# Kernel tuning notes

Measured on AMD Instinct MI355X. Metric: run time of the kernel, lower is better.

## Reference

```python
import jax, jax.numpy as jnp
from jax import lax
import numpy as np
import math

EPS = 1e-6

def _np(a, s=1.0):
    return np.asarray(a, dtype=np.float32) * np.float32(s)

def _gabor(theta, sigma=1.1, lambd=3.0, gamma=0.65):
    c = np.arange(-2, 3, dtype=np.float32)
    yy, xx = np.meshgrid(c, c, indexing='ij')
    xt = xx * math.cos(theta) + yy * math.sin(theta)
    yt = -xx * math.sin(theta) + yy * math.cos(theta)
    k = np.exp(-(xt**2 + gamma**2 * yt**2) / (2.0 * sigma**2)) * np.cos(2.0 * math.pi * xt / lambd)
    k = k - k.mean()
    return (k / max(np.abs(k).sum(), 1e-6)).astype(np.float32)

def _dct_like(u=2, v=2, size=5):
    c = np.arange(size, dtype=np.float32)
    yy, xx = np.meshgrid(c, c, indexing='ij')
    k = np.cos(math.pi*(2*xx+1)*u/(2*size)) * np.cos(math.pi*(2*yy+1)*v/(2*size))
    k = k - k.mean()
    return (k / max(np.abs(k).sum(), 1e-6)).astype(np.float32)

# stacked 3x3 stencils: laplacian, hess_xx, hess_yy, hess_xy, sobel_x, sobel_y, diag_main, diag_anti, checkerboard
_K3 = np.stack([
    _np([[0,1,0],[1,-4,1],[0,1,0]]),
    _np([[0,0,0],[1,-2,1],[0,0,0]]),
    _np([[0,1,0],[0,-2,0],[0,1,0]]),
    _np([[1,0,-1],[0,0,0],[-1,0,1]], 0.25),
    _np([[-1,0,1],[-2,0,2],[-1,0,1]], 0.125),
    _np([[-1,-2,-1],[0,0,0],[1,2,1]], 0.125),
    _np([[-2,-1,0],[-1,0,1],[0,1,2]], 0.125),
    _np([[0,1,2],[-1,0,1],[-2,-1,0]], 0.125),
    _np([[1,-1,1],[-1,1,-1],[1,-1,1]], 1.0/9.0),
])[:, None]

_Z5 = np.zeros((5,5), np.float32)

def _row5(vals):
    k = _Z5.copy(); k[2, :] = vals; return k

def _col5(vals):
    k = _Z5.copy(); k[:, 2] = vals; return k

# stacked 5x5 stencils: ha_second_h, ha_second_v, ha_green_h, ha_green_v, mhc_green, stripe_x, stripe_y, gabor45, gabor135, dct
_K5 = np.stack([
    _row5([-0.5, 0.0, 1.0, 0.0, -0.5]),
    _col5([-0.5, 0.0, 1.0, 0.0, -0.5]),
    _row5([-0.25, 0.5, 0.5, 0.5, -0.25]),
    _col5([-0.25, 0.5, 0.5, 0.5, -0.25]),
    _np([[0,0,-1,0,0],[0,0,2,0,0],[-1,2,4,2,-1],[0,0,2,0,0],[0,0,-1,0,0]], 0.125),
    _row5([0.25, -1.0, 1.5, -1.0, 0.25]),
    _col5([0.25, -1.0, 1.5, -1.0, 0.25]),
    _gabor(math.pi/4.0),
    _gabor(3.0*math.pi/4.0),
    _dct_like(),
])[:, None]

_SMOOTH5 = (_np([[1,2,3,2,1],[2,4,6,4,2],[3,6,9,6,3],[2,4,6,4,2],[1,2,3,2,1]]) / np.float32(81.0))[None, None]

K3 = jnp.asarray(_K3)
K5 = jnp.asarray(_K5)
SMOOTH5 = jnp.asarray(_SMOOTH5)

def _masks(H, W):
    # gbrg pattern
    z = lambda: np.zeros((1, 1, H, W), np.float32)
    r, b, gr, gb, row, col = z(), z(), z(), z(), z(), z()
    row[:, :, 1::2, :] = 1.0
    col[:, :, :, 1::2] = 1.0
    gb[:, :, 0::2, 0::2] = 1.0
    b[:, :, 0::2, 1::2] = 1.0
    r[:, :, 1::2, 0::2] = 1.0
    gr[:, :, 1::2, 1::2] = 1.0
    g = gr + gb
    return tuple(jnp.asarray(a) for a in (r, g, b, gr, gb, row, col))

def _pad(x, ph, pw):
    return jnp.pad(x, ((0, 0), (0, 0), (ph, ph), (pw, pw)), mode='reflect')

def _conv_same(x, k, groups=1):
    kh, kw = k.shape[-2:]
    return lax.conv_general_dilated(_pad(x, kh // 2, kw // 2), k.astype(x.dtype), (1, 1), 'VALID',
                                    dimension_numbers=('NCHW', 'OIHW', 'NCHW'),
                                    feature_group_count=groups)

def _avg_same(x, kh, kw):
    k = jnp.full((1, 1, kh, kw), 1.0 / (kh * kw), x.dtype)
    return _conv_same(x, k)

def _forward(bayer):
    B, _, H, W = bayer.shape
    r, g, b, gr, gb, row, col = _masks(H, W)
    c3 = _conv_same(bayer, K3)  # [B,9,H,W]
    lap, hxx, hyy, hxy, gx, gy, gdm, gda, chk = jnp.split(c3, 9, axis=1)
    c5 = _conv_same(bayer, K5)  # [B,10,H,W]
    hsh, hsv, hgh, hgv, mhcf, stx, sty, g45, g135, dctp = jnp.split(c5, 10, axis=1)
    # morphological gradient: 3x3 max - min (reflect-padded)
    xp = _pad(bayer, 1, 1)
    mgrad = (lax.reduce_window(xp, -jnp.inf, lax.max, (1, 1, 3, 3), (1, 1, 1, 1), 'VALID')
             - lax.reduce_window(xp, jnp.inf, lax.min, (1, 1, 3, 3), (1, 1, 1, 1), 'VALID'))
    gmag = jnp.sqrt(gx * gx + gy * gy + EPS)
    # structure tensor (3x3 box smoothing of gradient outer products)
    jxx = _avg_same(gx * gx, 3, 3)
    jyy = _avg_same(gy * gy, 3, 3)
    jxy = _avg_same(gx * gy, 3, 3)
    tr = jxx + jyy
    lam_gap = jnp.sqrt((jxx - jyy) ** 2 + 4.0 * jxy * jxy + EPS)
    coherence = lam_gap / (tr + EPS)
    anisotropy = (jxx - jyy) / (tr + EPS)
    ha_dis = jnp.abs(hgh - hgv)
    res_h = bayer - hgh
    res_v = bayer - hgv
    res_eh = _avg_same(res_h * res_h, 3, 3)
    res_ev = _avg_same(res_v * res_v, 3, 3)
    dgd = jnp.abs(gx) - jnp.abs(gy)
    dsd = jnp.abs(hxx) - jnp.abs(hyy)
    # 1x5 / 5x1 line variances
    mh = _avg_same(bayer, 1, 5)
    mv = _avg_same(bayer, 5, 1)
    lvh = jnp.maximum(_avg_same(bayer * bayer, 1, 5) - mh * mh, 0.0)
    lvv = jnp.maximum(_avg_same(bayer * bayer, 5, 1) - mv * mv, 0.0)
    lvd = lvh - lvv
    dconf = jnp.abs(lvd) / (lvh + lvv + EPS)
    # normalized sparse fills (smooth5 of masked signal / smooth5 of mask)
    mstack = jnp.concatenate([r, g, b, gr, gb], axis=1)  # [1,5,H,W]
    sig = bayer * mstack  # [B,5,H,W]
    ks = jnp.tile(SMOOTH5, (5, 1, 1, 1))
    num = _conv_same(sig, ks, groups=5)
    den = jnp.maximum(_conv_same(mstack, ks, groups=5), EPS)
    rf, gf, bf, grf, gbf = jnp.split(num / den, 5, axis=1)
    rg = rf - gf
    bg = bf - gf
    gpd = grf - gbf
    mhc = jnp.where(g > 0.5, bayer, mhcf)
    mhc_ha = mhc - 0.5 * (hgh + hgv)
    rres = (bayer - mhc) * r
    bres = (bayer - mhc) * b
    chk_e = _avg_same(chk * chk, 3, 3)
    str_e = _avg_same(stx * stx + sty * sty, 3, 3)
    lmean = _avg_same(bayer, 3, 3)
    lvar = jnp.maximum(_avg_same(bayer * bayer, 3, 3) - lmean * lmean, 0.0)
    gen = _avg_same(gx * gx + gy * gy, 3, 3)
    bm = lambda m: jnp.broadcast_to(m, bayer.shape)
    feats = [bm(r), bm(g), bm(b), bm(gr), bm(gb), bm(row), bm(col),
             lap, hxx, hyy, hxy, mgrad, gx, gy, gdm, gda, gmag,
             coherence, anisotropy, hsh, hsv, hgh, hgv, ha_dis,
             res_h, res_v, res_eh, res_ev, dgd, dsd, lvh, lvv, lvd, dconf,
             rg, bg, gpd, mhc, mhc_ha, rres, bres,
             stx, sty, chk, g45, g135, dctp, chk_e, str_e, lmean, lvar, gen]
    return jnp.concatenate(feats, axis=1)  # [B,52,H,W]

def setup_inputs() -> dict:
    key = jax.random.key(0)
    bayer = jax.random.uniform(key, (2, 1, 768, 768), dtype=jnp.float32)
    return {"bayer": bayer}

def reference(bayer):
    return _forward(bayer)
```

## Files before the change

### kernel.cpp

```cpp
#include <hip/hip_runtime.h>
#include <math.h>

#define H_ 768
#define W_ 768
#define TY 8
#define TX 64
#define NTHREADS 128
#define EPS_ 1e-6f

typedef float f4 __attribute__((ext_vector_type(4)));
typedef _Float16 h2 __attribute__((ext_vector_type(2)));

__device__ __forceinline__ f4 mk4(float x, float y, float z, float w){ f4 r; r.x=x; r.y=y; r.z=z; r.w=w; return r; }
__device__ __forceinline__ f4 sp(float s){ return mk4(s,s,s,s); }
__device__ __forceinline__ f4 max4(f4 a, f4 b){ return mk4(fmaxf(a.x,b.x),fmaxf(a.y,b.y),fmaxf(a.z,b.z),fmaxf(a.w,b.w)); }
__device__ __forceinline__ f4 sqrt4(f4 a){ return mk4(sqrtf(a.x),sqrtf(a.y),sqrtf(a.z),sqrtf(a.w)); }
__device__ __forceinline__ f4 abs4(f4 a){ return mk4(fabsf(a.x),fabsf(a.y),fabsf(a.z),fabsf(a.w)); }
__device__ __forceinline__ float rcp1(float x){
#if __has_builtin(__builtin_amdgcn_rcpf)
    return __builtin_amdgcn_rcpf(x);
#else
    return 1.0f / x;
#endif
}
__device__ __forceinline__ f4 rcp4(f4 a){ return mk4(rcp1(a.x),rcp1(a.y),rcp1(a.z),rcp1(a.w)); }
__device__ __forceinline__ h2 pk(float a, float b){ h2 r; r.x = (_Float16)a; r.y = (_Float16)b; return r; }

__device__ __forceinline__ int refl(int c, int n) {
    c = c < 0 ? -c : c;
    return c >= n ? 2 * n - 2 - c : c;
}

__global__ __launch_bounds__(NTHREADS, 4)
void bayer_feat(const float* __restrict__ in, float* __restrict__ out) {
    const int bz  = blockIdx.z;
    const int gy0 = blockIdx.y * TY;
    const int gx0 = blockIdx.x * TX;
    const int tid = threadIdx.x;
    const float* src = in + (size_t)bz * (H_ * W_);

    __shared__ float sB[TY + 6][TX + 7];
    __shared__ h2 sP[3][TY + 2][TX + 3];

    for (int i = tid; i < (TY + 6) * (TX + 6); i += NTHREADS) {
        int r = i / (TX + 6), c = i - r * (TX + 6);
        sB[r][c] = src[refl(gy0 - 3 + r, H_) * W_ + refl(gx0 - 3 + c, W_)];
    }
    __syncthreads();

    for (int i = tid; i < (TY + 2) * (TX + 2); i += NTHREADS) {
        int ey = i / (TX + 2), ex = i - ey * (TX + 2);
        int sy = refl(gy0 - 1 + ey, H_) - gy0 + 3;
        int sx = refl(gx0 - 1 + ex, W_) - gx0 + 3;
        float a00 = sB[sy-1][sx-1], a01 = sB[sy-1][sx], a02 = sB[sy-1][sx+1];
        float a10 = sB[sy  ][sx-1], a11 = sB[sy  ][sx], a12 = sB[sy  ][sx+1];
        float a20 = sB[sy+1][sx-1], a21 = sB[sy+1][sx], a22 = sB[sy+1][sx+1];
        float l2 = sB[sy][sx-2], r2 = sB[sy][sx+2];
        float u2 = sB[sy-2][sx], d2 = sB[sy+2][sx];
        float gx  = 0.125f * (-a00 + a02 - 2.f*a10 + 2.f*a12 - a20 + a22);
        float gy  = 0.125f * (-a00 - 2.f*a01 - a02 + a20 + 2.f*a21 + a22);
        float hgh = -0.25f*(l2 + r2) + 0.5f*(a10 + a11 + a12);
        float hgv = -0.25f*(u2 + d2) + 0.5f*(a01 + a11 + a21);
        float chk = (a00 - a01 + a02 - a10 + a11 - a12 + a20 - a21 + a22) * (1.f/9.f);
        float stx = 0.25f*(l2 + r2) - (a10 + a12) + 1.5f*a11;
        float sty = 0.25f*(u2 + d2) - (a01 + a21) + 1.5f*a11;
        float rh = a11 - hgh, rv = a11 - hgv;
        sP[0][ey][ex] = pk(gx, gy);
        sP[1][ey][ex] = pk(rh*rh, rv*rv);
        sP[2][ey][ex] = pk(chk*chk, stx*stx + sty*sty);
    }
    __syncthreads();

    const int lq  = tid & 15;
    const int ly  = tid >> 4;
    const int lx4 = lq * 4;
    const int gy  = gy0 + ly;
    const int py  = gy & 1;
    const int syc = ly + 3;
    const int ey  = ly + 1;
    const int exb = lx4 + 1;
    const size_t HW = (size_t)H_ * W_;
    float* po = out + (size_t)bz * 52 * HW + (size_t)gy * W_ + (gx0 + lx4);

#define ST(c, v) *(f4*)(po + (size_t)(c) * HW) = (v)
#define AV(r, i) mk4(a[r][i], a[r][(i)+1], a[r][(i)+2], a[r][(i)+3])

    const f4 zero4 = sp(0.f);
    const f4 ev01  = mk4(0,1,0,1);
    const f4 ev10  = mk4(1,0,1,0);
    const float inv9 = 1.f / 9.f;

    float a[5][8];
#pragma unroll
    for (int r = 0; r < 5; ++r)
#pragma unroll
        for (int i = 0; i < 8; ++i)
            a[r][i] = sB[syc - 2 + r][lx4 + 1 + i];


    {
        const float G45[5][5] = {
            {-0.002092f, -0.015195f, -0.063321f, -0.002285f,  0.036511f},
            {-0.015195f, -0.086304f,  0.003803f,  0.119456f, -0.002285f},
            {-0.063321f,  0.003803f,  0.172851f,  0.003803f, -0.063321f},
            {-0.002285f,  0.119456f,  0.003803f, -0.086304f, -0.015195f},
            { 0.036511f, -0.002285f, -0.063321f, -0.015195f, -0.002092f}
        };
        const float ADC[5] = {0.25f, -0.09549150f, -0.30901699f, -0.09549150f, 0.25f};
        f4 s45 = zero4, s135 = zero4, dct = zero4;
#pragma unroll
        for (int r = 0; r < 5; ++r) {
            f4 t = zero4;
#pragma unroll
            for (int i = 0; i < 5; ++i) {
                f4 v = AV(r, i);
                s45  += sp(G45[r][i])     * v;
                s135 += sp(G45[r][4 - i]) * v;
                t    += sp(ADC[i])        * v;
            }
            dct += sp(ADC[r]) * t;
        }
        ST(44, s45); ST(45, s135); ST(46, dct);
    }

    {
        f4 t0 = zero4, t1 = zero4, t2 = zero4, t3 = zero4;
#pragma unroll
        for (int r = 0; r < 5; ++r) {
            f4 E = AV(r,0) + sp(3.f)*AV(r,2) + AV(r,4);
            f4 O = sp(2.f)*(AV(r,1) + AV(r,3));
            f4 rE = mk4(E.x, O.y, E.z, O.w);
            f4 rO = mk4(O.x, E.y, O.z, E.w);
            if (r == 0 || r == 4)      { t0 += rE;          t2 += rO; }
            else if (r == 2)           { t0 += sp(3.f)*rE;  t2 += sp(3.f)*rO; }
            else                       { t1 += sp(2.f)*rE;  t3 += sp(2.f)*rO; }
        }
        f4 cEE = py ? t1 : t0, cOE = py ? t0 : t1, cEO = py ? t3 : t2, cOO = py ? t2 : t3;
        const f4 inv_r  = py ? mk4(0.04f,0.05f,0.04f,0.05f)     : mk4(0.05f,0.0625f,0.05f,0.0625f);
        const f4 inv_b  = py ? mk4(0.0625f,0.05f,0.0625f,0.05f) : mk4(0.05f,0.04f,0.05f,0.04f);
        const f4 inv_gr = py ? mk4(0.05f,0.04f,0.05f,0.04f)     : mk4(0.0625f,0.05f,0.0625f,0.05f);
        const f4 inv_gb = py ? mk4(0.05f,0.0625f,0.05f,0.0625f) : mk4(0.04f,0.05f,0.04f,0.05f);
        const f4 inv_g  = py ? mk4(1.f/40.f,1.f/41.f,1.f/40.f,1.f/41.f)
                             : mk4(1.f/41.f,1.f/40.f,1.f/41.f,1.f/40.f);
        f4 rfv = cOE*inv_r, bfv = cEO*inv_b, grfv = cOO*inv_gr, gbfv = cEE*inv_gb;
        f4 gfv = (cEE + cOO)*inv_g;
        ST(34, rfv - gfv); ST(35, bfv - gfv); ST(36, grfv - gbfv);
    }

    f4 ctr = AV(2,2);

    {
        f4 sh = AV(2,0)+AV(2,1)+ctr+AV(2,3)+AV(2,4);
        f4 qh = AV(2,0)*AV(2,0)+AV(2,1)*AV(2,1)+ctr*ctr+AV(2,3)*AV(2,3)+AV(2,4)*AV(2,4);
        f4 sv_ = AV(0,2)+AV(1,2)+ctr+AV(3,2)+AV(4,2);
        f4 qv_ = AV(0,2)*AV(0,2)+AV(1,2)*AV(1,2)+ctr*ctr+AV(3,2)*AV(3,2)+AV(4,2)*AV(4,2);
        f4 mh = sh * sp(0.2f), mv = sv_ * sp(0.2f);
        f4 lvh = max4(qh*sp(0.2f) - mh*mh, zero4);
        f4 lvv = max4(qv_*sp(0.2f) - mv*mv, zero4);
        ST(30, lvh); ST(31, lvv);
        f4 lvd = lvh - lvv;
        ST(32, lvd);
        ST(33, abs4(lvd) * rcp4(lvh + lvv + sp(EPS_)));
    }

    ST(19, sp(-0.5f)*(AV(2,0) + AV(2,4)) + ctr);
    ST(20, sp(-0.5f)*(AV(0,2) + AV(4,2)) + ctr);

    f4 hghc = sp(-0.25f)*(AV(2,0) + AV(2,4)) + sp(0.5f)*(AV(2,1) + ctr + AV(2,3));
    f4 hgvc = sp(-0.25f)*(AV(0,2) + AV(4,2)) + sp(0.5f)*(AV(1,2) + ctr + AV(3,2));
    {
        f4 mhcf = sp(0.125f)*( -AV(0,2) + sp(2.f)*AV(1,2) - AV(2,0) + sp(2.f)*AV(2,1) + sp(4.f)*ctr
                               + sp(2.f)*AV(2,3) - AV(2,4) + sp(2.f)*AV(3,2) - AV(4,2) );
        f4 mhc = py ? mk4(mhcf.x, ctr.y, mhcf.z, ctr.w) : mk4(ctr.x, mhcf.y, ctr.z, mhcf.w);
        ST(37, mhc);
        ST(38, mhc - sp(0.5f)*(hghc + hgvc));
        f4 dif = ctr - mhc;
        ST(39, dif * (py ? ev10 : zero4));
        ST(40, dif * (py ? zero4 : ev01));
    }
    ST(21, hghc); ST(22, hgvc);
    ST(23, abs4(hghc - hgvc));
    ST(24, ctr - hghc); ST(25, ctr - hgvc);

    {
        f4 gxc = sp(0.125f)*(-AV(1,1) + AV(1,3) - sp(2.f)*AV(2,1) + sp(2.f)*AV(2,3) - AV(3,1) + AV(3,3));
        f4 gyc = sp(0.125f)*(-AV(1,1) - sp(2.f)*AV(1,2) - AV(1,3) + AV(3,1) + sp(2.f)*AV(3,2) + AV(3,3));
        ST(12, gxc); ST(13, gyc);
        ST(16, sqrt4(gxc*gxc + gyc*gyc + sp(EPS_)));
        ST(28, abs4(gxc) - abs4(gyc));
    }
    {
        f4 stxc = sp(0.25f)*(AV(2,0) + AV(2,4)) - (AV(2,1) + AV(2,3)) + sp(1.5f)*ctr;
        f4 styc = sp(0.25f)*(AV(0,2) + AV(4,2)) - (AV(1,2) + AV(3,2)) + sp(1.5f)*ctr;
        f4 chkc = (AV(1,1) - AV(1,2) + AV(1,3) - AV(2,1) + ctr - AV(2,3) + AV(3,1) - AV(3,2) + AV(3,3)) * sp(inv9);
        ST(41, stxc); ST(42, styc); ST(43, chkc);
    }

    {
        f4 lap = AV(1,2) + AV(2,1) - sp(4.f)*ctr + AV(2,3) + AV(3,2);
        f4 hxx = AV(2,1) - sp(2.f)*ctr + AV(2,3);
        f4 hyy = AV(1,2) - sp(2.f)*ctr + AV(3,2);
        f4 hxy = sp(0.25f)*(AV(1,1) - AV(1,3) - AV(3,1) + AV(3,3));
        ST(7, lap); ST(8, hxx); ST(9, hyy); ST(10, hxy);
        ST(29, abs4(hxx) - abs4(hyy));
    }
    ST(14, sp(0.125f)*(sp(-2.f)*AV(1,1) - AV(1,2) - AV(2,1) + AV(2,3) + AV(3,2) + sp(2.f)*AV(3,3)));
    ST(15, sp(0.125f)*(AV(1,2) + sp(2.f)*AV(1,3) - AV(2,1) + AV(2,3) - sp(2.f)*AV(3,1) - AV(3,2)));

    {
        f4 mx = AV(1,1), mn = mx, s3 = zero4, q3 = zero4;
#pragma unroll
        for (int r = 1; r <= 3; ++r)
#pragma unroll
            for (int i = 1; i <= 3; ++i) {
                f4 v = AV(r,i);
                mx = max4(mx, v);
                mn = mk4(fminf(mn.x,v.x),fminf(mn.y,v.y),fminf(mn.z,v.z),fminf(mn.w,v.w));
                s3 += v; q3 += v*v;
            }
        ST(11, mx - mn);
        f4 lmean = s3 * sp(inv9);
        ST(49, lmean);
        ST(50, max4(q3*sp(inv9) - lmean*lmean, zero4));
    }

    {
        f4 jxx = zero4, jyy = zero4, jxy = zero4, reh = zero4, rev = zero4, cke = zero4, ste = zero4;
#pragma unroll
        for (int dy = -1; dy <= 1; ++dy) {
            float g_[6], h_[6];
#pragma unroll
            for (int j = 0; j < 6; ++j) {
                h2 v0 = sP[0][ey+dy][exb-1+j];
                g_[j] = (float)v0.x; h_[j] = (float)v0.y;
                h2 v1 = sP[1][ey+dy][exb-1+j];
                h2 v2 = sP[2][ey+dy][exb-1+j];
                (void)v1; (void)v2;
            }
#pragma unroll
            for (int o = 0; o < 3; ++o) {
                f4 q = mk4(g_[o], g_[o+1], g_[o+2], g_[o+3]);
                f4 w = mk4(h_[o], h_[o+1], h_[o+2], h_[o+3]);
                jxx += q*q; jyy += w*w; jxy += q*w;
            }
            float r2_[6], v2_[6], c2_[6], ss_[6];
#pragma unroll
            for (int j = 0; j < 6; ++j) {
                h2 v1 = sP[1][ey+dy][exb-1+j];
                r2_[j] = (float)v1.x; v2_[j] = (float)v1.y;
                h2 v2 = sP[2][ey+dy][exb-1+j];
                c2_[j] = (float)v2.x; ss_[j] = (float)v2.y;
            }
#pragma unroll
            for (int o = 0; o < 3; ++o) {
                reh += mk4(r2_[o], r2_[o+1], r2_[o+2], r2_[o+3]);
                rev += mk4(v2_[o], v2_[o+1], v2_[o+2], v2_[o+3]);
                cke += mk4(c2_[o], c2_[o+1], c2_[o+2], c2_[o+3]);
                ste += mk4(ss_[o], ss_[o+1], ss_[o+2], ss_[o+3]);
            }
        }
        jxx = jxx * sp(inv9); jyy = jyy * sp(inv9); jxy = jxy * sp(inv9);
        f4 trc = jxx + jyy;
        f4 dj  = jxx - jyy;
        f4 lam = sqrt4(dj*dj + sp(4.f)*jxy*jxy + sp(EPS_));
        f4 itr = rcp4(trc + sp(EPS_));
        ST(17, lam * itr);
        ST(18, dj * itr);
        ST(51, trc);
        ST(26, reh * sp(inv9)); ST(27, rev * sp(inv9));
        ST(47, cke * sp(inv9)); ST(48, ste * sp(inv9));
    }

    ST(0, py ? ev10 : zero4);
    ST(1, py ? ev01 : ev10);
    ST(2, py ? zero4 : ev01);
    ST(3, py ? ev01 : zero4);
    ST(4, py ? zero4 : ev10);
    ST(5, sp((float)py));
    ST(6, ev01);

#undef ST
#undef AV
}

extern "C" void kernel_launch(void* const* d_in, const int* in_sizes, int n_in,
                              void* d_out, int out_size, void* d_ws, size_t ws_size,
                              hipStream_t stream) {
    (void)n_in; (void)d_ws; (void)ws_size; (void)out_size;
    const float* bayer = (const float*)d_in[0];
    float* out = (float*)d_out;
    const int B = in_sizes[0] / (H_ * W_);
    dim3 grid(W_ / TX, H_ / TY, B);
    bayer_feat<<<grid, NTHREADS, 0, stream>>>(bayer, out);
}
```

Measured before the change: 47.53 us.

## Enlarge tile to 16x128 with 512 threads and vectorize shared-memory loads

Grows the block tile from 8x64 to 16x128 and the block from 128 to 512 threads, which cuts the fraction of halo pixels loaded and recomputed per output. Shared arrays are re-padded and offset so that 16-byte vector loads (f4 for the raw tile, h8 for the packed intermediates) are aligned, replacing scalar LDS reads. The larger block raises shared-memory use per block and may lower occupancy; launch_bounds still request 4 blocks per CU at 512 threads, which may constrain registers.

```diff
diff --git a/kernel.cpp b/kernel.cpp
--- a/kernel.cpp
+++ b/kernel.cpp
@@ -3,13 +3,17 @@
 
 #define H_ 768
 #define W_ 768
-#define TY 8
-#define TX 64
-#define NTHREADS 128
+#define TY 16
+#define TX 128
+#define NTHREADS 512
 #define EPS_ 1e-6f
+
+#define SBW 140
+#define SPW 132
 
 typedef float f4 __attribute__((ext_vector_type(4)));
 typedef _Float16 h2 __attribute__((ext_vector_type(2)));
+typedef _Float16 h8 __attribute__((ext_vector_type(8)));
 
 __device__ __forceinline__ f4 mk4(float x, float y, float z, float w){ f4 r; r.x=x; r.y=y; r.z=z; r.w=w; return r; }
 __device__ __forceinline__ f4 sp(float s){ return mk4(s,s,s,s); }
@@ -39,19 +43,19 @@
     const int tid = threadIdx.x;
     const float* src = in + (size_t)bz * (H_ * W_);
 
-    __shared__ float sB[TY + 6][TX + 7];
-    __shared__ h2 sP[3][TY + 2][TX + 3];
+    __shared__ __align__(16) float sB[TY + 6][SBW];
+    __shared__ __align__(16) h2 sP[3][TY + 2][SPW];
 
     for (int i = tid; i < (TY + 6) * (TX + 6); i += NTHREADS) {
         int r = i / (TX + 6), c = i - r * (TX + 6);
-        sB[r][c] = src[refl(gy0 - 3 + r, H_) * W_ + refl(gx0 - 3 + c, W_)];
+        sB[r][c + 3] = src[refl(gy0 - 3 + r, H_) * W_ + refl(gx0 - 3 + c, W_)];
     }
     __syncthreads();
 
     for (int i = tid; i < (TY + 2) * (TX + 2); i += NTHREADS) {
         int ey = i / (TX + 2), ex = i - ey * (TX + 2);
         int sy = refl(gy0 - 1 + ey, H_) - gy0 + 3;
-        int sx = refl(gx0 - 1 + ex, W_) - gx0 + 3;
+        int sx = refl(gx0 - 1 + ex, W_) - gx0 + 6;
         float a00 = sB[sy-1][sx-1], a01 = sB[sy-1][sx], a02 = sB[sy-1][sx+1];
         float a10 = sB[sy  ][sx-1], a11 = sB[sy  ][sx], a12 = sB[sy  ][sx+1];
         float a20 = sB[sy+1][sx-1], a21 = sB[sy+1][sx], a22 = sB[sy+1][sx+1];
@@ -71,14 +75,13 @@
     }
     __syncthreads();
 
-    const int lq  = tid & 15;
-    const int ly  = tid >> 4;
+    const int lq  = tid & 31;
+    const int ly  = tid >> 5;
     const int lx4 = lq * 4;
     const int gy  = gy0 + ly;
     const int py  = gy & 1;
     const int syc = ly + 3;
     const int ey  = ly + 1;
-    const int exb = lx4 + 1;
     const size_t HW = (size_t)H_ * W_;
     float* po = out + (size_t)bz * 52 * HW + (size_t)gy * W_ + (gx0 + lx4);
 
@@ -92,10 +95,12 @@
 
     float a[5][8];
 #pragma unroll
-    for (int r = 0; r < 5; ++r)
-#pragma unroll
-        for (int i = 0; i < 8; ++i)
-            a[r][i] = sB[syc - 2 + r][lx4 + 1 + i];
+    for (int r = 0; r < 5; ++r) {
+        f4 lo = *(const f4*)&sB[syc - 2 + r][lx4 + 4];
+        f4 hi = *(const f4*)&sB[syc - 2 + r][lx4 + 8];
+        a[r][0]=lo.x; a[r][1]=lo.y; a[r][2]=lo.z; a[r][3]=lo.w;
+        a[r][4]=hi.x; a[r][5]=hi.y; a[r][6]=hi.z; a[r][7]=hi.w;
+    }
 
 
     {
@@ -228,31 +233,34 @@
         f4 jxx = zero4, jyy = zero4, jxy = zero4, reh = zero4, rev = zero4, cke = zero4, ste = zero4;
 #pragma unroll
         for (int dy = -1; dy <= 1; ++dy) {
-            float g_[6], h_[6];
-#pragma unroll
-            for (int j = 0; j < 6; ++j) {
-                h2 v0 = sP[0][ey+dy][exb-1+j];
-                g_[j] = (float)v0.x; h_[j] = (float)v0.y;
-                h2 v1 = sP[1][ey+dy][exb-1+j];
-                h2 v2 = sP[2][ey+dy][exb-1+j];
-                (void)v1; (void)v2;
+            const int ry = ey + dy;
+            float g_[6], h_[6], r2_[6], v2_[6], c2_[6], ss_[6];
+            {
+                const h8 e = *(const h8*)&sP[0][ry][lx4];
+                g_[0]=e[0]; h_[0]=e[1]; g_[1]=e[2]; h_[1]=e[3];
+                g_[2]=e[4]; h_[2]=e[5]; g_[3]=e[6]; h_[3]=e[7];
+                h2 a4 = sP[0][ry][lx4+4], a5 = sP[0][ry][lx4+5];
+                g_[4]=a4.x; h_[4]=a4.y; g_[5]=a5.x; h_[5]=a5.y;
+            }
+            {
+                const h8 e = *(const h8*)&sP[1][ry][lx4];
+                r2_[0]=e[0]; v2_[0]=e[1]; r2_[1]=e[2]; v2_[1]=e[3];
+                r2_[2]=e[4]; v2_[2]=e[5]; r2_[3]=e[6]; v2_[3]=e[7];
+                h2 a4 = sP[1][ry][lx4+4], a5 = sP[1][ry][lx4+5];
+                r2_[4]=a4.x; v2_[4]=a4.y; r2_[5]=a5.x; v2_[5]=a5.y;
+            }
+            {
+                const h8 e = *(const h8*)&sP[2][ry][lx4];
+                c2_[0]=e[0]; ss_[0]=e[1]; c2_[1]=e[2]; ss_[1]=e[3];
+                c2_[2]=e[4]; ss_[2]=e[5]; c2_[3]=e[6]; ss_[3]=e[7];
+                h2 a4 = sP[2][ry][lx4+4], a5 = sP[2][ry][lx4+5];
+                c2_[4]=a4.x; ss_[4]=a4.y; c2_[5]=a5.x; ss_[5]=a5.y;
             }
 #pragma unroll
             for (int o = 0; o < 3; ++o) {
                 f4 q = mk4(g_[o], g_[o+1], g_[o+2], g_[o+3]);
                 f4 w = mk4(h_[o], h_[o+1], h_[o+2], h_[o+3]);
                 jxx += q*q; jyy += w*w; jxy += q*w;
-            }
-            float r2_[6], v2_[6], c2_[6], ss_[6];
-#pragma unroll
-            for (int j = 0; j < 6; ++j) {
-                h2 v1 = sP[1][ey+dy][exb-1+j];
-                r2_[j] = (float)v1.x; v2_[j] = (float)v1.y;
-                h2 v2 = sP[2][ey+dy][exb-1+j];
-                c2_[j] = (float)v2.x; ss_[j] = (float)v2.y;
-            }
-#pragma unroll
-            for (int o = 0; o < 3; ++o) {
                 reh += mk4(r2_[o], r2_[o+1], r2_[o+2], r2_[o+3]);
                 rev += mk4(v2_[o], v2_[o+1], v2_[o+2], v2_[o+3]);
                 cke += mk4(c2_[o], c2_[o+1], c2_[o+2], c2_[o+3]);
```

After: 50.71 us. 1.07x slower.

## Double tile height, raise occupancy bound, and split stencil accumulations to cut registers

Applied to the files above, without the earlier changes.

Doubles the tile height to 16 rows with 256 threads per block, which amortizes the 3-pixel halo loads over more output rows. It raises the launch-bounds minimum blocks per SM from 4 to 6. The shared-memory box-filter accumulations are split into three separate scopes with narrower live ranges, and the hghc/hgvc temporaries move into an inner scope. The aim is lower register pressure so the higher occupancy target fits, at the risk of register spills and larger shared memory per block.

```diff
diff --git a/kernel.cpp b/kernel.cpp
--- a/kernel.cpp
+++ b/kernel.cpp
@@ -3,9 +3,9 @@
 
 #define H_ 768
 #define W_ 768
-#define TY 8
+#define TY 16
 #define TX 64
-#define NTHREADS 128
+#define NTHREADS 256
 #define EPS_ 1e-6f
 
 typedef float f4 __attribute__((ext_vector_type(4)));
@@ -31,7 +31,7 @@
     return c >= n ? 2 * n - 2 - c : c;
 }
 
-__global__ __launch_bounds__(NTHREADS, 4)
+__global__ __launch_bounds__(NTHREADS, 6)
 void bayer_feat(const float* __restrict__ in, float* __restrict__ out) {
     const int bz  = blockIdx.z;
     const int gy0 = blockIdx.y * TY;
@@ -166,9 +166,9 @@
     ST(19, sp(-0.5f)*(AV(2,0) + AV(2,4)) + ctr);
     ST(20, sp(-0.5f)*(AV(0,2) + AV(4,2)) + ctr);
 
-    f4 hghc = sp(-0.25f)*(AV(2,0) + AV(2,4)) + sp(0.5f)*(AV(2,1) + ctr + AV(2,3));
-    f4 hgvc = sp(-0.25f)*(AV(0,2) + AV(4,2)) + sp(0.5f)*(AV(1,2) + ctr + AV(3,2));
-    {
+    {
+        f4 hghc = sp(-0.25f)*(AV(2,0) + AV(2,4)) + sp(0.5f)*(AV(2,1) + ctr + AV(2,3));
+        f4 hgvc = sp(-0.25f)*(AV(0,2) + AV(4,2)) + sp(0.5f)*(AV(1,2) + ctr + AV(3,2));
         f4 mhcf = sp(0.125f)*( -AV(0,2) + sp(2.f)*AV(1,2) - AV(2,0) + sp(2.f)*AV(2,1) + sp(4.f)*ctr
                                + sp(2.f)*AV(2,3) - AV(2,4) + sp(2.f)*AV(3,2) - AV(4,2) );
         f4 mhc = py ? mk4(mhcf.x, ctr.y, mhcf.z, ctr.w) : mk4(ctr.x, mhcf.y, ctr.z, mhcf.w);
@@ -177,10 +177,10 @@
         f4 dif = ctr - mhc;
         ST(39, dif * (py ? ev10 : zero4));
         ST(40, dif * (py ? zero4 : ev01));
-    }
-    ST(21, hghc); ST(22, hgvc);
-    ST(23, abs4(hghc - hgvc));
-    ST(24, ctr - hghc); ST(25, ctr - hgvc);
+        ST(21, hghc); ST(22, hgvc);
+        ST(23, abs4(hghc - hgvc));
+        ST(24, ctr - hghc); ST(25, ctr - hgvc);
+    }
 
     {
         f4 gxc = sp(0.125f)*(-AV(1,1) + AV(1,3) - sp(2.f)*AV(2,1) + sp(2.f)*AV(2,3) - AV(3,1) + AV(3,3));
@@ -225,38 +225,56 @@
     }
 
     {
-        f4 jxx = zero4, jyy = zero4, jxy = zero4, reh = zero4, rev = zero4, cke = zero4, ste = zero4;
+        f4 reh = zero4, rev = zero4;
+#pragma unroll
+        for (int dy = -1; dy <= 1; ++dy) {
+            float r2_[6], v2_[6];
+#pragma unroll
+            for (int j = 0; j < 6; ++j) {
+                h2 v = sP[1][ey+dy][exb-1+j];
+                r2_[j] = (float)v.x; v2_[j] = (float)v.y;
+            }
+#pragma unroll
+            for (int o = 0; o < 3; ++o) {
+                reh += mk4(r2_[o], r2_[o+1], r2_[o+2], r2_[o+3]);
+                rev += mk4(v2_[o], v2_[o+1], v2_[o+2], v2_[o+3]);
+            }
+        }
+        ST(26, reh * sp(inv9)); ST(27, rev * sp(inv9));
+    }
+    {
+        f4 cke = zero4, ste = zero4;
+#pragma unroll
+        for (int dy = -1; dy <= 1; ++dy) {
+            float c2_[6], ss_[6];
+#pragma unroll
+            for (int j = 0; j < 6; ++j) {
+                h2 v = sP[2][ey+dy][exb-1+j];
+                c2_[j] = (float)v.x; ss_[j] = (float)v.y;
+            }
+#pragma unroll
+            for (int o = 0; o < 3; ++o) {
+                cke += mk4(c2_[o], c2_[o+1], c2_[o+2], c2_[o+3]);
+                ste += mk4(ss_[o], ss_[o+1], ss_[o+2], ss_[o+3]);
+            }
+        }
+        ST(47, cke * sp(inv9)); ST(48, ste * sp(inv9));
+    }
+    {
+        f4 jxx = zero4, jyy = zero4, jxy = zero4;
 #pragma unroll
         for (int dy = -1; dy <= 1; ++dy) {
             float g_[6], h_[6];
 #pragma unroll
             for (int j = 0; j < 6; ++j) {
-                h2 v0 = sP[0][ey+dy][exb-1+j];
-                g_[j] = (float)v0.x; h_[j] = (float)v0.y;
-                h2 v1 = sP[1][ey+dy][exb-1+j];
-                h2 v2 = sP[2][ey+dy][exb-1+j];
-                (void)v1; (void)v2;
+                h2 v = sP[0][ey+dy][exb-1+j];
+                g_[j] = (float)v.x; h_[j] = (float)v.y;
             }
 #pragma unroll
             for (int o = 0; o < 3; ++o) {
                 f4 q = mk4(g_[o], g_[o+1], g_[o+2], g_[o+3]);
                 f4 w = mk4(h_[o], h_[o+1], h_[o+2], h_[o+3]);
                 jxx += q*q; jyy += w*w; jxy += q*w;
-            }
-            float r2_[6], v2_[6], c2_[6], ss_[6];
-#pragma unroll
-            for (int j = 0; j < 6; ++j) {
-                h2 v1 = sP[1][ey+dy][exb-1+j];
-                r2_[j] = (float)v1.x; v2_[j] = (float)v1.y;
-                h2 v2 = sP[2][ey+dy][exb-1+j];
-                c2_[j] = (float)v2.x; ss_[j] = (float)v2.y;
-            }
-#pragma unroll
-            for (int o = 0; o < 3; ++o) {
-                reh += mk4(r2_[o], r2_[o+1], r2_[o+2], r2_[o+3]);
-                rev += mk4(v2_[o], v2_[o+1], v2_[o+2], v2_[o+3]);
-                cke += mk4(c2_[o], c2_[o+1], c2_[o+2], c2_[o+3]);
-                ste += mk4(ss_[o], ss_[o+1], ss_[o+2], ss_[o+3]);
             }
         }
         jxx = jxx * sp(inv9); jyy = jyy * sp(inv9); jxy = jxy * sp(inv9);
@@ -267,8 +285,6 @@
         ST(17, lam * itr);
         ST(18, dj * itr);
         ST(51, trc);
-        ST(26, reh * sp(inv9)); ST(27, rev * sp(inv9));
-        ST(47, cke * sp(inv9)); ST(48, ste * sp(inv9));
     }
 
     ST(0, py ? ev10 : zero4);
```

Measured after the change: 58.78 us. 1.24x slower.
